# Kernel tuning notes

Measured on AMD Instinct MI355X. Metric: run time of the kernel, lower is better.

The kernel has to match this reference:

```python
import jax, jax.numpy as jnp
import numpy as np

KS = 7           # kernel spatial size (odd)
OMEGA0 = 10.0    # SIREN frequency
PAD = 3          # conv padding ('same' for ks=7)


def _rel_positions_grid(ks):
    # [2, ks, ks], coords in [-1, 1]
    lin = jnp.linspace(-1.0, 1.0, ks, dtype=jnp.float32)
    yy, xx = jnp.meshgrid(lin, lin, indexing='ij')
    return jnp.stack([yy, xx], axis=0)


def _siren(points, W1, b1, W2, b2, W3, b3):
    # points: [..., 3] -> [..., out_ch*in_ch]
    h = jnp.sin(OMEGA0 * (points @ W1 + b1))
    h = jnp.sin(OMEGA0 * (h @ W2 + b2))
    return h @ W3 + b3


def setup_inputs() -> dict:
    key = jax.random.key(0)
    ks = jax.random.split(key, 8)
    B, Cin, Cout, G, H, W, Hid = 16, 32, 32, 8, 64, 64, 32
    x = jax.random.normal(ks[0], (B, Cin, G, H, W), dtype=jnp.float32)
    # deterministic rotation grid on SO(2): angles in [0, 2pi)
    input_g_elems = (jnp.arange(G, dtype=jnp.float32) * (2.0 * jnp.pi / G))[None, :]
    # SIREN params: 3 -> Hid -> Hid -> Cout*Cin
    W1 = jax.random.uniform(ks[1], (3, Hid), minval=-1.0, maxval=1.0) / 3.0
    b1 = jnp.zeros((Hid,), jnp.float32)
    c = jnp.sqrt(6.0 / Hid) / OMEGA0
    W2 = jax.random.uniform(ks[2], (Hid, Hid), minval=-c, maxval=c)
    b2 = jnp.zeros((Hid,), jnp.float32)
    W3 = jax.random.uniform(ks[3], (Hid, Cout * Cin), minval=-c, maxval=c)
    b3 = jnp.zeros((Cout * Cin,), jnp.float32)
    bias = jnp.zeros((1, Cout), jnp.float32)
    return {"x": x, "input_g_elems": input_g_elems, "W1": W1, "b1": b1,
            "W2": W2, "b2": b2, "W3": W3, "b3": b3, "bias": bias}


def reference(x, input_g_elems, W1, b1, W2, b2, W3, b3, bias):
    B, Cin, Gin, H, Wd = x.shape
    Cout = bias.shape[1]
    two_pi = 2.0 * jnp.pi
    rel_pos = _rel_positions_grid(KS)                        # [2, ks, ks]

    # deterministic / non-partial path: g_elems = input_g_elems
    thetas = input_g_elems[0]                                # [G]
    Gout = thetas.shape[0]

    # acted group coords: inv(g) . h = (h - g) mod 2pi, normalized to [-1, 1)
    acted_g = jnp.mod(thetas[None, :] - thetas[:, None], two_pi) / jnp.pi - 1.0  # [Gout, Gin]

    # rotate Rd rel positions by inv(g) = R(-theta)
    ct, st = jnp.cos(-thetas), jnp.sin(-thetas)
    R = jnp.stack([jnp.stack([ct, -st], -1), jnp.stack([st, ct], -1)], -2)  # [Gout,2,2]
    acted_rel = jnp.einsum('gij,jhw->gihw', R, rel_pos)      # [Gout,2,ks,ks]

    # positions fed to kernel net: [Gout, Gin, ks, ks, 3]
    pos_rd = jnp.broadcast_to(acted_rel[:, :, None], (Gout, 2, Gin, KS, KS))
    pos_g = jnp.broadcast_to(acted_g[:, None, :, None, None], (Gout, 1, Gin, KS, KS))
    coords = jnp.concatenate([pos_rd, pos_g], axis=1)        # [Gout,3,Gin,ks,ks]
    points = jnp.moveaxis(coords, 1, -1)                     # [Gout,Gin,ks,ks,3]

    kernel = _siren(points, W1, b1, W2, b2, W3, b3)          # [Gout,Gin,ks,ks,Cout*Cin]
    kernel = kernel.reshape(Gout, Gin, KS, KS, Cout, Cin)
    kernel = jnp.transpose(kernel, (0, 4, 5, 1, 2, 3))       # [Gout,Cout,Cin,Gin,ks,ks]

    # zero kernel outside unit disk of (rotated) Rd positions
    mask = (jnp.linalg.norm(acted_rel, axis=1) <= 1.0)       # [Gout,ks,ks]
    kernel = kernel * mask[:, None, None, None, :, :]

    weight = kernel.reshape(Gout * Cout, Cin * Gin, KS, KS)
    x2 = x.reshape(B, Cin * Gin, H, Wd)
    out = jax.lax.conv_general_dilated(
        x2, weight, window_strides=(1, 1), padding=[(PAD, PAD), (PAD, PAD)],
        dimension_numbers=('NCHW', 'OIHW', 'NCHW'))          # [B, Gout*Cout, H, W]
    out = out.reshape(B, Gout, Cout, H, Wd).transpose(0, 2, 1, 3, 4)  # [B,Cout,Gout,H,W]
    out = out + bias.reshape(1, Cout, 1, 1, 1)
    return out
```

## Files before the change

### kernel.cpp

```cpp
#include <hip/hip_runtime.h>
#include <math.h>

typedef __bf16 bf16_t;
typedef __bf16 bf16x8 __attribute__((ext_vector_type(8)));
typedef float  f32x4  __attribute__((ext_vector_type(4)));

#define B_    16
#define CIN_  32
#define COUT_ 32
#define G_    8
#define CH_   256
#define H_    64
#define W_    64
#define HID_  32
#define KS_   7
#define PAD_  3
#define WP_   70

#define ROW_ELEMS  (WP_ * CH_)
#define XP_ELEMS   ((size_t)B_ * WP_ * ROW_ELEMS)
#define XP_BYTES   (XP_ELEMS * 2)

#define REPACK_BLOCKS (B_ * (H_ + 6))
#define GENW_BLOCKS   (G_ * G_)
#define CONV_BLOCKS   (B_ * (H_ / 2))

static __device__ __forceinline__ unsigned pack_bf16(float a, float b) {
    union { __bf16 h; unsigned short u; } ua, ub;
    ua.h = (__bf16)a; ub.h = (__bf16)b;
    return (unsigned)ua.u | ((unsigned)ub.u << 16);
}

static __device__ __forceinline__ void dma16(const bf16_t* g, bf16_t* l) {
    __builtin_amdgcn_global_load_lds(
        (const __attribute__((address_space(1))) void*)g,
        (__attribute__((address_space(3))) void*)l, 16, 0, 0);
}

__global__ void prep(const float* __restrict__ x, bf16_t* __restrict__ xp,
                     const float* __restrict__ thetas,
                     const float* __restrict__ W1, const float* __restrict__ b1,
                     const float* __restrict__ W2, const float* __restrict__ b2,
                     const float* __restrict__ W3, const float* __restrict__ b3,
                     bf16_t* __restrict__ w2out) {
    __shared__ float h1s[49][33];
    __shared__ float h2s[49][33];
    __shared__ float masks[49];
    int tid = threadIdx.x;
    if (blockIdx.x < REPACK_BLOCKS) {
        int blk = blockIdx.x;
        int b = blk / (H_ + 6), hy = blk % (H_ + 6);
        const int4 z4 = make_int4(0, 0, 0, 0);
        if (hy >= H_) {
            int idx = hy - H_;
            int y = (idx < 3) ? idx : idx + 64;
            bf16_t* dst = xp + ((size_t)(b * WP_) + y) * ROW_ELEMS;
            for (int i = tid; i < ROW_ELEMS / 8; i += 256)
                *reinterpret_cast<int4*>(dst + (size_t)i * 8) = z4;
            return;
        }
        int lane = tid & 63, wv = tid >> 6;
        int r = lane >> 3;
        int t = lane & 7;
        size_t orow = ((size_t)(b * WP_) + (hy + 3)) * ROW_ELEMS;
        for (int it = 0; it < 8; ++it) {
            int c0 = wv * 8 + it * 32;
            const float* src = x + ((size_t)(b * CH_ + c0 + r)) * (H_ * W_)
                                 + (size_t)hy * W_ + t * 8;
            float4 f0 = *reinterpret_cast<const float4*>(src);
            float4 f1 = *reinterpret_cast<const float4*>(src + 4);
            int d0 = (int)pack_bf16(f0.x, f0.y);
            int d1 = (int)pack_bf16(f0.z, f0.w);
            int d2 = (int)pack_bf16(f1.x, f1.y);
            int d3 = (int)pack_bf16(f1.z, f1.w);
            int p0, p1, p2, p3;
            p0 = __shfl_xor(d0, 32); p1 = __shfl_xor(d1, 32);
            p2 = __shfl_xor(d2, 32); p3 = __shfl_xor(d3, 32);
            if ((r & 4) == 0) { d2 = p0; d3 = p1; } else { d0 = p2; d1 = p3; }
            p0 = __shfl_xor(d0, 16); p1 = __shfl_xor(d1, 16);
            p2 = __shfl_xor(d2, 16); p3 = __shfl_xor(d3, 16);
            if ((r & 2) == 0) { d1 = p0; d3 = p2; } else { d0 = p1; d2 = p3; }
            p0 = __shfl_xor(d0, 8); p1 = __shfl_xor(d1, 8);
            p2 = __shfl_xor(d2, 8); p3 = __shfl_xor(d3, 8);
            if ((r & 1) == 0) {
                d0 = (d0 & 0xFFFF) | (p0 << 16);
                d1 = (d1 & 0xFFFF) | (p1 << 16);
                d2 = (d2 & 0xFFFF) | (p2 << 16);
                d3 = (d3 & 0xFFFF) | (p3 << 16);
            } else {
                d0 = (d0 & 0xFFFF0000) | ((unsigned)p0 >> 16);
                d1 = (d1 & 0xFFFF0000) | ((unsigned)p1 >> 16);
                d2 = (d2 & 0xFFFF0000) | ((unsigned)p2 >> 16);
                d3 = (d3 & 0xFFFF0000) | ((unsigned)p3 >> 16);
            }
            int xpos = t * 8 + r + 3;
            int c16 = c0 >> 3;
            int4 v = make_int4(d0, d1, d2, d3);
            *reinterpret_cast<int4*>(xp + orow + ((size_t)c16 * WP_ + xpos) * 8) = v;
        }
        if (tid < 192) {
            int col = tid >> 5, cg = tid & 31;
            int xx = (col < 3) ? col : col + 64;
            *reinterpret_cast<int4*>(xp + orow + ((size_t)cg * WP_ + xx) * 8) = z4;
        }
        return;
    }
    int blk = blockIdx.x - REPACK_BLOCKS;
    int gin = blk & 7, gout = blk >> 3;
    const float TWO_PI = 6.283185307179586f;
    const float PI_F   = 3.14159265358979323846f;
    float th_o = thetas[gout], th_i = thetas[gin];
    float d = fmodf(th_i - th_o, TWO_PI);
    if (d < 0.0f) d += TWO_PI;
    float ag = d / PI_F - 1.0f;
    float ct = cosf(-th_o), st = sinf(-th_o);

    if (tid < 196) {
        int p = tid >> 2, q = tid & 3;
        int ky = p / 7, kx = p % 7;
        float yy = (float)(ky - 3) / 3.0f;
        float xx = (float)(kx - 3) / 3.0f;
        float r0 = ct * yy - st * xx;
        float r1 = st * yy + ct * xx;
        if (q == 0)
            masks[p] = (r0 * r0 + r1 * r1 <= 1.00001f) ? 1.0f : 0.0f;
        #pragma unroll
        for (int jo = 0; jo < 8; ++jo) {
            int j = q * 8 + jo;
            float a = r0 * W1[j] + r1 * W1[32 + j] + ag * W1[64 + j] + b1[j];
            h1s[p][j] = __sinf(10.0f * a);
        }
    }
    __syncthreads();
    if (tid < 196) {
        int p = tid >> 2, q = tid & 3;
        #pragma unroll
        for (int jo = 0; jo < 8; ++jo) {
            int j = q * 8 + jo;
            float a = b2[j];
            #pragma unroll
            for (int i = 0; i < HID_; ++i) a += h1s[p][i] * W2[i * HID_ + j];
            h2s[p][j] = __sinf(10.0f * a);
        }
    }
    __syncthreads();
    for (int rep = 0; rep < 4; ++rep) {
        int o = rep * 256 + tid;
        float w3c[HID_];
        #pragma unroll
        for (int i = 0; i < HID_; ++i) w3c[i] = W3[i * 1024 + o];
        float bb = b3[o];
        int cout = o >> 5, cin = o & 31;
        int k = cin * G_ + gin;
        int n = gout * COUT_ + cout;
        int kc = k >> 5, hi = (k >> 3) & 3, jj = k & 7;
        bf16_t* dst = w2out + (((size_t)kc * 4 + hi) * 256 + n) * 8 + jj;
        for (int p = 0; p < 49; ++p) {
            float a = bb;
            #pragma unroll
            for (int i = 0; i < HID_; ++i) a += h2s[p][i] * w3c[i];
            a *= masks[p];
            dst[(size_t)p * (8 * 4 * 256 * 8)] = (bf16_t)a;
        }
    }
}

__launch_bounds__(256, 2)
__global__ void conv_mfma(const bf16_t* __restrict__ xp,
                          const bf16_t* __restrict__ w2,
                          const float* __restrict__ bias,
                          float* __restrict__ out) {
    __shared__ __align__(16) bf16_t lds[2][ROW_ELEMS];
    int blk = blockIdx.x;
    int b = blk >> 5, h0 = (blk & 31) << 1;
    int tid = threadIdx.x;
    int ns = tid >> 6, lane = tid & 63;
    int lm = lane & 15, lq = lane >> 4;

    f32x4 acc[8][4];
    #pragma unroll
    for (int i = 0; i < 8; ++i)
        #pragma unroll
        for (int j = 0; j < 4; ++j) {
            f32x4 z = {0.0f, 0.0f, 0.0f, 0.0f};
            acc[i][j] = z;
        }

    const bf16_t* rows = xp + (((size_t)(b * WP_) + h0)) * ROW_ELEMS;
    for (int c = ns; c < 70; c += 4)
        dma16(rows + (size_t)c * 512 + lane * 8, &lds[0][0] + c * 512);
    __syncthreads();

    for (int ky = 0; ky < KS_; ++ky) {
        const bf16_t* slotA = &lds[ky & 1][0];
        const bf16_t* slotB = &lds[(ky + 1) & 1][0];
        #pragma unroll 1
        for (int kx = 0; kx < KS_; ++kx) {
            int tap = ky * KS_ + kx;
            const bf16_t* wbase = w2 + ((size_t)(tap * 32 + lq) * 256 + (ns * 64 + lm)) * 8;
            #pragma unroll 2
            for (int kc = 0; kc < 8; ++kc) {
                const bf16_t* wp = wbase + (size_t)kc * (4 * 256 * 8);
                bf16x8 bfrag[4];
                #pragma unroll
                for (int nt = 0; nt < 4; ++nt)
                    bfrag[nt] = *reinterpret_cast<const bf16x8*>(wp + nt * (16 * 8));
                int cb = (kc * 4 + lq) * WP_;
                bf16x8 afrag[8];
                #pragma unroll
                for (int mt = 0; mt < 4; ++mt) {
                    int xr = mt * 16 + lm + kx;
                    afrag[mt]     = *reinterpret_cast<const bf16x8*>(&slotA[(cb + xr) * 8]);
                    afrag[mt + 4] = *reinterpret_cast<const bf16x8*>(&slotB[(cb + xr) * 8]);
                }
                #pragma unroll
                for (int mt = 0; mt < 8; ++mt)
                    #pragma unroll
                    for (int nt = 0; nt < 4; ++nt)
                        acc[mt][nt] = __builtin_amdgcn_mfma_f32_16x16x32_bf16(
                            afrag[mt], bfrag[nt], acc[mt][nt], 0, 0, 0);
            }
        }
        if (ky < KS_ - 1) {
            __syncthreads();
            bf16_t* dstslot = &lds[ky & 1][0];
            const bf16_t* src = rows + (size_t)(ky + 2) * ROW_ELEMS;
            for (int c = ns; c < 35; c += 4)
                dma16(src + (size_t)c * 512 + lane * 8, dstslot + c * 512);
            __syncthreads();
        }
    }

    #pragma unroll
    for (int mt = 0; mt < 8; ++mt) {
        int h = h0 + (mt >> 2);
        int wq = (mt & 3) * 16 + lq * 4;
        #pragma unroll
        for (int nt = 0; nt < 4; ++nt) {
            int n = ns * 64 + nt * 16 + lm;
            int gout = n >> 5, cout = n & 31;
            float bv = bias[cout];
            f32x4 v = acc[mt][nt];
            v[0] += bv; v[1] += bv; v[2] += bv; v[3] += bv;
            float* po = out + (((size_t)(b * COUT_ + cout) * G_ + gout) * (H_ * W_)
                               + h * W_ + wq);
            *reinterpret_cast<f32x4*>(po) = v;
        }
    }
}

extern "C" void kernel_launch(void* const* d_in, const int* in_sizes, int n_in,
                              void* d_out, int out_size, void* d_ws, size_t ws_size,
                              hipStream_t stream) {
    const float* x      = (const float*)d_in[0];
    const float* thetas = (const float*)d_in[1];
    const float* W1     = (const float*)d_in[2];
    const float* b1     = (const float*)d_in[3];
    const float* W2     = (const float*)d_in[4];
    const float* b2     = (const float*)d_in[5];
    const float* W3     = (const float*)d_in[6];
    const float* b3     = (const float*)d_in[7];
    const float* bias   = (const float*)d_in[8];
    float* out = (float*)d_out;

    bf16_t* xp = (bf16_t*)d_ws;
    bf16_t* w2 = (bf16_t*)((char*)d_ws + XP_BYTES);

    hipLaunchKernelGGL(prep, dim3(REPACK_BLOCKS + GENW_BLOCKS), dim3(256), 0, stream,
                       x, xp, thetas, W1, b1, W2, b2, W3, b3, w2);
    hipLaunchKernelGGL(conv_mfma, dim3(CONV_BLOCKS), dim3(256), 0, stream,
                       xp, w2, bias, out);
}
```

Baseline: 477.7 us.

## Register-prefetch conv weight fragments and repartition SIREN weight generation per tap

The conv inner loop is flattened into a 56-step sequence per kernel row, and the B-weight fragments for the next step are loaded into a second register set while the current step's MFMAs run. This is meant to hide global-load latency on the weight reads. The weight-generation blocks change from one per (gout, gin) pair to one per (gout, tap). Each thread now writes 8 gin values as a single 16-byte vector store instead of scattered 2-byte stores, and these blocks are scheduled before the repack blocks. The cost is extra register pressure under launch_bounds(256,2) and more generation blocks, each doing a smaller amount of work.

```diff
diff --git a/kernel.cpp b/kernel.cpp
--- a/kernel.cpp
+++ b/kernel.cpp
@@ -21,8 +21,8 @@
 #define XP_ELEMS   ((size_t)B_ * WP_ * ROW_ELEMS)
 #define XP_BYTES   (XP_ELEMS * 2)
 
+#define GENW_BLOCKS   (G_ * KS_ * KS_)
 #define REPACK_BLOCKS (B_ * (H_ + 6))
-#define GENW_BLOCKS   (G_ * G_)
 #define CONV_BLOCKS   (B_ * (H_ / 2))
 
 static __device__ __forceinline__ unsigned pack_bf16(float a, float b) {
@@ -43,127 +43,145 @@
                      const float* __restrict__ W2, const float* __restrict__ b2,
                      const float* __restrict__ W3, const float* __restrict__ b3,
                      bf16_t* __restrict__ w2out) {
-    __shared__ float h1s[49][33];
-    __shared__ float h2s[49][33];
-    __shared__ float masks[49];
+    __shared__ float h1s[8][33];
+    __shared__ float h2s[8][33];
     int tid = threadIdx.x;
-    if (blockIdx.x < REPACK_BLOCKS) {
+    if (blockIdx.x < GENW_BLOCKS) {
         int blk = blockIdx.x;
-        int b = blk / (H_ + 6), hy = blk % (H_ + 6);
-        const int4 z4 = make_int4(0, 0, 0, 0);
-        if (hy >= H_) {
-            int idx = hy - H_;
-            int y = (idx < 3) ? idx : idx + 64;
-            bf16_t* dst = xp + ((size_t)(b * WP_) + y) * ROW_ELEMS;
-            for (int i = tid; i < ROW_ELEMS / 8; i += 256)
-                *reinterpret_cast<int4*>(dst + (size_t)i * 8) = z4;
-            return;
-        }
-        int lane = tid & 63, wv = tid >> 6;
-        int r = lane >> 3;
-        int t = lane & 7;
-        size_t orow = ((size_t)(b * WP_) + (hy + 3)) * ROW_ELEMS;
-        for (int it = 0; it < 8; ++it) {
-            int c0 = wv * 8 + it * 32;
-            const float* src = x + ((size_t)(b * CH_ + c0 + r)) * (H_ * W_)
-                                 + (size_t)hy * W_ + t * 8;
-            float4 f0 = *reinterpret_cast<const float4*>(src);
-            float4 f1 = *reinterpret_cast<const float4*>(src + 4);
-            int d0 = (int)pack_bf16(f0.x, f0.y);
-            int d1 = (int)pack_bf16(f0.z, f0.w);
-            int d2 = (int)pack_bf16(f1.x, f1.y);
-            int d3 = (int)pack_bf16(f1.z, f1.w);
-            int p0, p1, p2, p3;
-            p0 = __shfl_xor(d0, 32); p1 = __shfl_xor(d1, 32);
-            p2 = __shfl_xor(d2, 32); p3 = __shfl_xor(d3, 32);
-            if ((r & 4) == 0) { d2 = p0; d3 = p1; } else { d0 = p2; d1 = p3; }
-            p0 = __shfl_xor(d0, 16); p1 = __shfl_xor(d1, 16);
-            p2 = __shfl_xor(d2, 16); p3 = __shfl_xor(d3, 16);
-            if ((r & 2) == 0) { d1 = p0; d3 = p2; } else { d0 = p1; d2 = p3; }
-            p0 = __shfl_xor(d0, 8); p1 = __shfl_xor(d1, 8);
-            p2 = __shfl_xor(d2, 8); p3 = __shfl_xor(d3, 8);
-            if ((r & 1) == 0) {
-                d0 = (d0 & 0xFFFF) | (p0 << 16);
-                d1 = (d1 & 0xFFFF) | (p1 << 16);
-                d2 = (d2 & 0xFFFF) | (p2 << 16);
-                d3 = (d3 & 0xFFFF) | (p3 << 16);
-            } else {
-                d0 = (d0 & 0xFFFF0000) | ((unsigned)p0 >> 16);
-                d1 = (d1 & 0xFFFF0000) | ((unsigned)p1 >> 16);
-                d2 = (d2 & 0xFFFF0000) | ((unsigned)p2 >> 16);
-                d3 = (d3 & 0xFFFF0000) | ((unsigned)p3 >> 16);
-            }
-            int xpos = t * 8 + r + 3;
-            int c16 = c0 >> 3;
-            int4 v = make_int4(d0, d1, d2, d3);
-            *reinterpret_cast<int4*>(xp + orow + ((size_t)c16 * WP_ + xpos) * 8) = v;
-        }
-        if (tid < 192) {
-            int col = tid >> 5, cg = tid & 31;
-            int xx = (col < 3) ? col : col + 64;
-            *reinterpret_cast<int4*>(xp + orow + ((size_t)cg * WP_ + xx) * 8) = z4;
-        }
-        return;
-    }
-    int blk = blockIdx.x - REPACK_BLOCKS;
-    int gin = blk & 7, gout = blk >> 3;
-    const float TWO_PI = 6.283185307179586f;
-    const float PI_F   = 3.14159265358979323846f;
-    float th_o = thetas[gout], th_i = thetas[gin];
-    float d = fmodf(th_i - th_o, TWO_PI);
-    if (d < 0.0f) d += TWO_PI;
-    float ag = d / PI_F - 1.0f;
-    float ct = cosf(-th_o), st = sinf(-th_o);
-
-    if (tid < 196) {
-        int p = tid >> 2, q = tid & 3;
-        int ky = p / 7, kx = p % 7;
+        int gout = blk / 49, p = blk - gout * 49;
+        int ky = p / 7, kx = p - ky * 7;
+        const float TWO_PI = 6.283185307179586f;
+        const float PI_F   = 3.14159265358979323846f;
+        float th_o = thetas[gout];
+        float ct = cosf(-th_o), st = sinf(-th_o);
         float yy = (float)(ky - 3) / 3.0f;
         float xx = (float)(kx - 3) / 3.0f;
         float r0 = ct * yy - st * xx;
         float r1 = st * yy + ct * xx;
-        if (q == 0)
-            masks[p] = (r0 * r0 + r1 * r1 <= 1.00001f) ? 1.0f : 0.0f;
-        #pragma unroll
-        for (int jo = 0; jo < 8; ++jo) {
-            int j = q * 8 + jo;
+        float maskv = (r0 * r0 + r1 * r1 <= 1.00001f) ? 1.0f : 0.0f;
+
+        int gin = tid >> 5, j = tid & 31;
+        {
+            float th_i = thetas[gin];
+            float d = fmodf(th_i - th_o, TWO_PI);
+            if (d < 0.0f) d += TWO_PI;
+            float ag = d / PI_F - 1.0f;
             float a = r0 * W1[j] + r1 * W1[32 + j] + ag * W1[64 + j] + b1[j];
-            h1s[p][j] = __sinf(10.0f * a);
-        }
-    }
-    __syncthreads();
-    if (tid < 196) {
-        int p = tid >> 2, q = tid & 3;
-        #pragma unroll
-        for (int jo = 0; jo < 8; ++jo) {
-            int j = q * 8 + jo;
+            h1s[gin][j] = __sinf(10.0f * a);
+        }
+        __syncthreads();
+        {
             float a = b2[j];
             #pragma unroll
-            for (int i = 0; i < HID_; ++i) a += h1s[p][i] * W2[i * HID_ + j];
-            h2s[p][j] = __sinf(10.0f * a);
-        }
-    }
-    __syncthreads();
-    for (int rep = 0; rep < 4; ++rep) {
-        int o = rep * 256 + tid;
-        float w3c[HID_];
-        #pragma unroll
-        for (int i = 0; i < HID_; ++i) w3c[i] = W3[i * 1024 + o];
-        float bb = b3[o];
-        int cout = o >> 5, cin = o & 31;
-        int k = cin * G_ + gin;
-        int n = gout * COUT_ + cout;
-        int kc = k >> 5, hi = (k >> 3) & 3, jj = k & 7;
-        bf16_t* dst = w2out + (((size_t)kc * 4 + hi) * 256 + n) * 8 + jj;
-        for (int p = 0; p < 49; ++p) {
-            float a = bb;
+            for (int i = 0; i < HID_; ++i) a += h1s[gin][i] * W2[i * HID_ + j];
+            h2s[gin][j] = __sinf(10.0f * a);
+        }
+        __syncthreads();
+        for (int rep = 0; rep < 4; ++rep) {
+            int o = rep * 256 + tid;
+            float w3c[HID_];
             #pragma unroll
-            for (int i = 0; i < HID_; ++i) a += h2s[p][i] * w3c[i];
-            a *= masks[p];
-            dst[(size_t)p * (8 * 4 * 256 * 8)] = (bf16_t)a;
-        }
-    }
-}
+            for (int i = 0; i < HID_; ++i) w3c[i] = W3[i * 1024 + o];
+            float bb = b3[o];
+            int cout = o >> 5, cin = o & 31;
+            union { bf16x8 v; bf16_t e[8]; } o8;
+            #pragma unroll
+            for (int g = 0; g < 8; ++g) {
+                float a = bb;
+                #pragma unroll
+                for (int i = 0; i < HID_; ++i) a += h2s[g][i] * w3c[i];
+                o8.e[g] = (bf16_t)(a * maskv);
+            }
+            size_t base = ((size_t)p * 8192 + (size_t)cin * 256
+                           + (size_t)(gout * COUT_ + cout)) * 8;
+            *reinterpret_cast<bf16x8*>(w2out + base) = o8.v;
+        }
+        return;
+    }
+    int blk = blockIdx.x - GENW_BLOCKS;
+    int b = blk / (H_ + 6), hy = blk % (H_ + 6);
+    const int4 z4 = make_int4(0, 0, 0, 0);
+    if (hy >= H_) {
+        int idx = hy - H_;
+        int y = (idx < 3) ? idx : idx + 64;
+        bf16_t* dst = xp + ((size_t)(b * WP_) + y) * ROW_ELEMS;
+        for (int i = tid; i < ROW_ELEMS / 8; i += 256)
+            *reinterpret_cast<int4*>(dst + (size_t)i * 8) = z4;
+        return;
+    }
+    int lane = tid & 63, wv = tid >> 6;
+    int r = lane >> 3;
+    int t = lane & 7;
+    size_t orow = ((size_t)(b * WP_) + (hy + 3)) * ROW_ELEMS;
+    for (int it = 0; it < 8; ++it) {
+        int c0 = wv * 8 + it * 32;
+        const float* src = x + ((size_t)(b * CH_ + c0 + r)) * (H_ * W_)
+                             + (size_t)hy * W_ + t * 8;
+        float4 f0 = *reinterpret_cast<const float4*>(src);
+        float4 f1 = *reinterpret_cast<const float4*>(src + 4);
+        int d0 = (int)pack_bf16(f0.x, f0.y);
+        int d1 = (int)pack_bf16(f0.z, f0.w);
+        int d2 = (int)pack_bf16(f1.x, f1.y);
+        int d3 = (int)pack_bf16(f1.z, f1.w);
+        int p0, p1, p2, p3;
+        p0 = __shfl_xor(d0, 32); p1 = __shfl_xor(d1, 32);
+        p2 = __shfl_xor(d2, 32); p3 = __shfl_xor(d3, 32);
+        if ((r & 4) == 0) { d2 = p0; d3 = p1; } else { d0 = p2; d1 = p3; }
+        p0 = __shfl_xor(d0, 16); p1 = __shfl_xor(d1, 16);
+        p2 = __shfl_xor(d2, 16); p3 = __shfl_xor(d3, 16);
+        if ((r & 2) == 0) { d1 = p0; d3 = p2; } else { d0 = p1; d2 = p3; }
+        p0 = __shfl_xor(d0, 8); p1 = __shfl_xor(d1, 8);
+        p2 = __shfl_xor(d2, 8); p3 = __shfl_xor(d3, 8);
+        if ((r & 1) == 0) {
+            d0 = (d0 & 0xFFFF) | (p0 << 16);
+            d1 = (d1 & 0xFFFF) | (p1 << 16);
+            d2 = (d2 & 0xFFFF) | (p2 << 16);
+            d3 = (d3 & 0xFFFF) | (p3 << 16);
+        } else {
+            d0 = (d0 & 0xFFFF0000) | ((unsigned)p0 >> 16);
+            d1 = (d1 & 0xFFFF0000) | ((unsigned)p1 >> 16);
+            d2 = (d2 & 0xFFFF0000) | ((unsigned)p2 >> 16);
+            d3 = (d3 & 0xFFFF0000) | ((unsigned)p3 >> 16);
+        }
+        int xpos = t * 8 + r + 3;
+        int c16 = c0 >> 3;
+        int4 v = make_int4(d0, d1, d2, d3);
+        *reinterpret_cast<int4*>(xp + orow + ((size_t)c16 * WP_ + xpos) * 8) = v;
+    }
+    if (tid < 192) {
+        int col = tid >> 5, cg = tid & 31;
+        int xx = (col < 3) ? col : col + 64;
+        *reinterpret_cast<int4*>(xp + orow + ((size_t)cg * WP_ + xx) * 8) = z4;
+    }
+}
+
+#define CONV_STEP(USE, PRE, SS)                                               \
+  do {                                                                        \
+    int sl = (SS) + 1, kyn = ky;                                              \
+    if (sl == 56) { sl = 0; kyn = ky + 1; if (kyn == 7) { kyn = 6; sl = 55; } }\
+    int tapn = kyn * 7 + (sl >> 3), kcn = sl & 7;                             \
+    const bf16_t* wpn = w2 + ((size_t)(tapn * 32 + lq) * 256 + nbase) * 8     \
+                        + (size_t)kcn * (4 * 256 * 8);                        \
+    PRE[0] = *reinterpret_cast<const bf16x8*>(wpn);                           \
+    PRE[1] = *reinterpret_cast<const bf16x8*>(wpn + 128);                     \
+    PRE[2] = *reinterpret_cast<const bf16x8*>(wpn + 256);                     \
+    PRE[3] = *reinterpret_cast<const bf16x8*>(wpn + 384);                     \
+    int kx = (SS) >> 3, kc = (SS) & 7;                                        \
+    int cb = (kc * 4 + lq) * WP_;                                             \
+    bf16x8 afrag[8];                                                          \
+    _Pragma("unroll")                                                         \
+    for (int mt = 0; mt < 4; ++mt) {                                          \
+      int xr = mt * 16 + lm + kx;                                             \
+      afrag[mt]     = *reinterpret_cast<const bf16x8*>(&slotA[(cb + xr) * 8]);\
+      afrag[mt + 4] = *reinterpret_cast<const bf16x8*>(&slotB[(cb + xr) * 8]);\
+    }                                                                         \
+    _Pragma("unroll")                                                         \
+    for (int mt = 0; mt < 8; ++mt)                                            \
+      _Pragma("unroll")                                                       \
+      for (int nt = 0; nt < 4; ++nt)                                          \
+        acc[mt][nt] = __builtin_amdgcn_mfma_f32_16x16x32_bf16(                \
+            afrag[mt], USE[nt], acc[mt][nt], 0, 0, 0);                        \
+  } while (0)
 
 __launch_bounds__(256, 2)
 __global__ void conv_mfma(const bf16_t* __restrict__ xp,
@@ -176,6 +194,7 @@
     int tid = threadIdx.x;
     int ns = tid >> 6, lane = tid & 63;
     int lm = lane & 15, lq = lane >> 4;
+    int nbase = ns * 64 + lm;
 
     f32x4 acc[8][4];
     #pragma unroll
@@ -189,37 +208,24 @@
     const bf16_t* rows = xp + (((size_t)(b * WP_) + h0)) * ROW_ELEMS;
     for (int c = ns; c < 70; c += 4)
         dma16(rows + (size_t)c * 512 + lane * 8, &lds[0][0] + c * 512);
+
+    bf16x8 bcur[4], bnxt[4];
+    {
+        const bf16_t* wp0 = w2 + ((size_t)lq * 256 + nbase) * 8;
+        bcur[0] = *reinterpret_cast<const bf16x8*>(wp0);
+        bcur[1] = *reinterpret_cast<const bf16x8*>(wp0 + 128);
+        bcur[2] = *reinterpret_cast<const bf16x8*>(wp0 + 256);
+        bcur[3] = *reinterpret_cast<const bf16x8*>(wp0 + 384);
+    }
     __syncthreads();
 
     for (int ky = 0; ky < KS_; ++ky) {
         const bf16_t* slotA = &lds[ky & 1][0];
         const bf16_t* slotB = &lds[(ky + 1) & 1][0];
         #pragma unroll 1
-        for (int kx = 0; kx < KS_; ++kx) {
-            int tap = ky * KS_ + kx;
-            const bf16_t* wbase = w2 + ((size_t)(tap * 32 + lq) * 256 + (ns * 64 + lm)) * 8;
-            #pragma unroll 2
-            for (int kc = 0; kc < 8; ++kc) {
-                const bf16_t* wp = wbase + (size_t)kc * (4 * 256 * 8);
-                bf16x8 bfrag[4];
-                #pragma unroll
-                for (int nt = 0; nt < 4; ++nt)
-                    bfrag[nt] = *reinterpret_cast<const bf16x8*>(wp + nt * (16 * 8));
-                int cb = (kc * 4 + lq) * WP_;
-                bf16x8 afrag[8];
-                #pragma unroll
-                for (int mt = 0; mt < 4; ++mt) {
-                    int xr = mt * 16 + lm + kx;
-                    afrag[mt]     = *reinterpret_cast<const bf16x8*>(&slotA[(cb + xr) * 8]);
-                    afrag[mt + 4] = *reinterpret_cast<const bf16x8*>(&slotB[(cb + xr) * 8]);
-                }
-                #pragma unroll
-                for (int mt = 0; mt < 8; ++mt)
-                    #pragma unroll
-                    for (int nt = 0; nt < 4; ++nt)
-                        acc[mt][nt] = __builtin_amdgcn_mfma_f32_16x16x32_bf16(
-                            afrag[mt], bfrag[nt], acc[mt][nt], 0, 0, 0);
-            }
+        for (int s = 0; s < 56; s += 2) {
+            CONV_STEP(bcur, bnxt, s);
+            CONV_STEP(bnxt, bcur, s + 1);
         }
         if (ky < KS_ - 1) {
             __syncthreads();
@@ -266,7 +272,7 @@
     bf16_t* xp = (bf16_t*)d_ws;
     bf16_t* w2 = (bf16_t*)((char*)d_ws + XP_BYTES);
 
-    hipLaunchKernelGGL(prep, dim3(REPACK_BLOCKS + GENW_BLOCKS), dim3(256), 0, stream,
+    hipLaunchKernelGGL(prep, dim3(GENW_BLOCKS + REPACK_BLOCKS), dim3(256), 0, stream,
                        x, xp, thetas, W1, b1, W2, b2, W3, b3, w2);
     hipLaunchKernelGGL(conv_mfma, dim3(CONV_BLOCKS), dim3(256), 0, stream,
                        xp, w2, bias, out);
```

Result: slower. 544.9 us (+14.1%).
